# Performance work log

Hardware: AMD Instinct MI355X
Metric: run time of the kernel (lower is better)

Reference implementation:

```python
import jax, jax.numpy as jnp
import numpy as np

N_NODES = 100000
D = 128
R = 4
E = 150000


def setup_inputs() -> dict:
    key = jax.random.key(0)
    k1, k2, k3, k4, k5 = jax.random.split(key, 5)
    x = jax.random.normal(k1, (N_NODES, D), dtype=jnp.float32)
    src_idx = jax.random.randint(k2, (R, E), 0, N_NODES, dtype=jnp.int32)
    dst_idx = jax.random.randint(k3, (R, E), 0, N_NODES, dtype=jnp.int32)
    # xavier-ish scale for weights
    rel_weight = jax.random.normal(k4, (R, D, D), dtype=jnp.float32) * (2.0 / np.sqrt(D))
    loop_weight = jax.random.normal(k5, (D, D), dtype=jnp.float32) * (2.0 / np.sqrt(D))
    h_bias = jnp.zeros((D,), dtype=jnp.float32)
    return {"x": x, "src_idx": src_idx, "dst_idx": dst_idx,
            "rel_weight": rel_weight, "loop_weight": loop_weight, "h_bias": h_bias}


def reference(x, src_idx, dst_idx, rel_weight, loop_weight, h_bias):
    # Per-relation GraphConv with norm='right': gather src feats, scatter-sum to
    # dst, divide by in-degree (clamped to 1), then per-relation linear.
    n = x.shape[0]

    def one_rel(src, dst):
        agg = jax.ops.segment_sum(x[src], dst, num_segments=n)          # [N, D]
        deg = jax.ops.segment_sum(jnp.ones(dst.shape, x.dtype), dst, num_segments=n)
        return agg / jnp.maximum(deg, 1.0)[:, None]

    agg = jax.vmap(one_rel)(src_idx, dst_idx)                           # [R, N, D]
    h = jnp.einsum('rnd,rde->ne', agg, rel_weight)                      # sum over relations
    h = h + x @ loop_weight + h_bias                                    # self-loop + bias
    return jax.nn.relu(h)
```

## Files before the change

### kernel.cpp

```cpp
#include <hip/hip_runtime.h>

#define N_NODES 100000
#define D 128
#define R_REL 4
#define E_EDGES 150000
#define M_SEG (R_REL * N_NODES)
#define NSEG 5
#define CAP 16
#define PLANE ((size_t)N_NODES * D)

typedef _Float16 half8v __attribute__((ext_vector_type(8)));
typedef float f32x4 __attribute__((ext_vector_type(4)));

#define EB ((R_REL * E_EDGES + 255) / 256)
#define BCONV_N (NSEG * 4 * 8 * 64 * 8)
#define BB ((BCONV_N + 255) / 256)
#define XB ((N_NODES * 16 + 255) / 256)

__device__ __forceinline__ void gload_lds16(const void* g, void* l) {
    __builtin_amdgcn_global_load_lds(
        (const __attribute__((address_space(1))) unsigned int*)g,
        (__attribute__((address_space(3))) unsigned int*)l, 16, 0, 0);
}

__global__ __launch_bounds__(256) void prep_kernel(
    const int* __restrict__ src_idx, const int* __restrict__ dst_idx,
    const float* __restrict__ rel_w, const float* __restrict__ loop_w,
    const float* __restrict__ x,
    int* __restrict__ cnt, int* __restrict__ epool,
    _Float16* __restrict__ bh, _Float16* __restrict__ zall)
{
    if (blockIdx.x < EB) {
        int idx = blockIdx.x * 256 + threadIdx.x;
        if (idx >= R_REL * E_EDGES) return;
        int r = idx / E_EDGES;
        int i = r * N_NODES + dst_idx[idx];
        int pos = atomicAdd(&cnt[i], 1);
        if (pos < CAP) epool[(size_t)i * CAP + pos] = src_idx[idx];
    } else if (blockIdx.x < EB + BB) {
        int idx = (blockIdx.x - EB) * 256 + threadIdx.x;
        if (idx >= BCONV_N) return;
        int j   = idx & 7;
        int l   = (idx >> 3) & 63;
        int t   = (idx >> 9) & 7;
        int ks  = (idx >> 12) & 3;
        int seg = idx >> 14;
        int k   = ks * 32 + (l >> 4) * 8 + j;
        int col = t * 16 + (l & 15);
        float v = (seg < R_REL) ? rel_w[((size_t)seg * D + k) * D + col]
                                : loop_w[(size_t)k * D + col];
        bh[idx] = (_Float16)v;
    } else {
        int f = (blockIdx.x - EB - BB) * 256 + threadIdx.x;
        if (f >= N_NODES * 16) return;
        int n = f >> 4;
        int c = f & 15;
        const float4* x4 = (const float4*)x;
        float4 a = x4[(size_t)n * 32 + c * 2];
        float4 b = x4[(size_t)n * 32 + c * 2 + 1];
        half8v h = {(_Float16)a.x, (_Float16)a.y, (_Float16)a.z, (_Float16)a.w,
                    (_Float16)b.x, (_Float16)b.y, (_Float16)b.z, (_Float16)b.w};
        _Float16* xp = zall + (size_t)R_REL * PLANE;
        *(half8v*)(xp + (size_t)n * D + ((c ^ (n & 7)) * 8)) = h;
    }
}

__global__ __launch_bounds__(256) void aggh_kernel(
    const int* __restrict__ cnt,
    const int* __restrict__ epool,
    _Float16* __restrict__ zall)
{
    int idx = blockIdx.x * 256 + threadIdx.x;
    int sid = idx >> 4;
    int lane = idx & 15;
    if (sid >= M_SEG) return;
    int n = sid % N_NODES;

    const _Float16* xp = zall + (size_t)R_REL * PLANE;
    int c = cnt[sid];
    int cc = min(c, CAP);
    int4 i4 = ((const int4*)epool)[(size_t)sid * (CAP / 4)];

    int s0 = (0 < cc) ? i4.x : 0;  float m0 = (0 < cc) ? 1.f : 0.f;
    int s1 = (1 < cc) ? i4.y : 0;  float m1 = (1 < cc) ? 1.f : 0.f;
    int s2 = (2 < cc) ? i4.z : 0;  float m2 = (2 < cc) ? 1.f : 0.f;
    int s3 = (3 < cc) ? i4.w : 0;  float m3 = (3 < cc) ? 1.f : 0.f;
    half8v v0 = *(const half8v*)(xp + (size_t)s0 * D + ((lane ^ (s0 & 7)) * 8));
    half8v v1 = *(const half8v*)(xp + (size_t)s1 * D + ((lane ^ (s1 & 7)) * 8));
    half8v v2 = *(const half8v*)(xp + (size_t)s2 * D + ((lane ^ (s2 & 7)) * 8));
    half8v v3 = *(const half8v*)(xp + (size_t)s3 * D + ((lane ^ (s3 & 7)) * 8));

    float s[8];
    #pragma unroll
    for (int e = 0; e < 8; e++)
        s[e] = (float)v0[e] * m0 + (float)v1[e] * m1 +
               (float)v2[e] * m2 + (float)v3[e] * m3;

    for (int j = 4; j < cc; j++) {
        int sj = epool[(size_t)sid * CAP + j];
        half8v v = *(const half8v*)(xp + (size_t)sj * D + ((lane ^ (sj & 7)) * 8));
        #pragma unroll
        for (int e = 0; e < 8; e++) s[e] += (float)v[e];
    }

    float sc = 1.0f / fmaxf((float)c, 1.0f);
    half8v o;
    #pragma unroll
    for (int e = 0; e < 8; e++) o[e] = (_Float16)(s[e] * sc);
    *(half8v*)(zall + (size_t)sid * D + ((lane ^ (n & 7)) * 8)) = o;
}

__global__ __launch_bounds__(256) void gemm_kernel(
    const _Float16* __restrict__ zall,
    const _Float16* __restrict__ bh,
    const float* __restrict__ bias,
    float* __restrict__ out)
{
    __shared__ __align__(16) char lds[64 * 528];

    int tid = threadIdx.x;
    int w = tid >> 6;
    int l = tid & 63;
    int n0 = blockIdx.x * 64;

    f32x4 acc[8];
    #pragma unroll
    for (int t = 0; t < 8; t++) acc[t] = (f32x4){0.f, 0.f, 0.f, 0.f};

    int arow = w * 16 + (l & 15);

    for (int seg = 0; seg < NSEG; seg++) {
        const char* plane = (const char*)(zall + (size_t)seg * PLANE)
                          + (size_t)n0 * 256;
        #pragma unroll
        for (int p = 0; p < 4; p++) {
            int f = p * 256 + tid;
            gload_lds16(plane + f * 16, lds + f * 16);
        }
        __syncthreads();

        half8v aF[4];
        #pragma unroll
        for (int ks = 0; ks < 4; ks++) {
            int cbyte = (ks * 64 + ((l >> 4) << 4)) ^ ((arow & 7) << 4);
            aF[ks] = *(const half8v*)(lds + arow * 256 + cbyte);
        }
        #pragma unroll
        for (int ks = 0; ks < 4; ks++) {
            size_t fb = ((((size_t)seg * 4 + ks) * 8) * 64 + l) * 8;
            #pragma unroll
            for (int t = 0; t < 8; t++) {
                half8v bF = *(const half8v*)(bh + fb + (size_t)t * 512);
                acc[t] = __builtin_amdgcn_mfma_f32_16x16x32_f16(aF[ks], bF, acc[t], 0, 0, 0);
            }
        }
        __syncthreads();
    }

    int cl = l & 15;
    int lrow0 = w * 16 + ((l >> 4) << 2);
    #pragma unroll
    for (int t = 0; t < 8; t++) {
        float bv = bias[t * 16 + cl];
        #pragma unroll
        for (int reg = 0; reg < 4; reg++) {
            float v = fmaxf(acc[t][reg] + bv, 0.f);
            ((float*)(lds + (lrow0 + reg) * 528))[t * 16 + cl] = v;
        }
    }
    __syncthreads();
    #pragma unroll
    for (int p = 0; p < 8; p++) {
        int f = p * 256 + tid;
        int row = f >> 5;
        int s = f & 31;
        float4 rv = *(const float4*)(lds + row * 528 + s * 16);
        int n = n0 + row;
        if (n < N_NODES)
            *(float4*)((char*)(out + (size_t)n * D) + s * 16) = rv;
    }
}

extern "C" void kernel_launch(void* const* d_in, const int* in_sizes, int n_in,
                              void* d_out, int out_size, void* d_ws, size_t ws_size,
                              hipStream_t stream)
{
    const float* x      = (const float*)d_in[0];
    const int*   src    = (const int*)d_in[1];
    const int*   dst    = (const int*)d_in[2];
    const float* rel_w  = (const float*)d_in[3];
    const float* loop_w = (const float*)d_in[4];
    const float* bias   = (const float*)d_in[5];
    float* out = (float*)d_out;

    int* cnt   = (int*)d_ws;
    int* epool = cnt + M_SEG;
    _Float16* bh = (_Float16*)(epool + (size_t)M_SEG * CAP);
    size_t zoff = ((size_t)M_SEG * 4 + (size_t)M_SEG * CAP * 4 +
                   (size_t)BCONV_N * 2 + 255) & ~(size_t)255;
    _Float16* zall = (_Float16*)((char*)d_ws + zoff);

    hipMemsetAsync(cnt, 0, (size_t)M_SEG * sizeof(int), stream);
    prep_kernel<<<EB + BB + XB, 256, 0, stream>>>(src, dst, rel_w, loop_w, x,
                                                  cnt, epool, bh, zall);

    const int ablocks = (M_SEG * 16) / 256;
    aggh_kernel<<<ablocks, 256, 0, stream>>>(cnt, epool, zall);

    const int gblocks = (N_NODES + 63) / 64;
    gemm_kernel<<<gblocks, 256, 0, stream>>>(zall, bh, bias, out);
}
```

Before: 238.2 us.

## Double-buffer GEMM A tiles, widen block to 128 rows, skip empty segments

The GEMM kernel now handles 128 rows per block, with each wave computing two 16-row tiles that share every loaded B fragment. It prefetches the next segment's A plane into a second LDS buffer while the current one is consumed, so global loads overlap with MFMA work. The epilogue writes its results in two halves through LDS. The aggregation kernel adds an early exit that writes zeros for segments with no edges, which skips the index and gather loads for them. Trade-offs: more LDS and accumulator registers, which can lower occupancy, and half as many GEMM blocks.

Measured after the change: 252.1 us. 5.8% more time.

```diff
diff --git a/kernel.cpp b/kernel.cpp
--- a/kernel.cpp
+++ b/kernel.cpp
@@ -76,12 +76,20 @@
     if (sid >= M_SEG) return;
     int n = sid % N_NODES;
 
+    int c = cnt[sid];
+    _Float16* op = zall + (size_t)sid * D + ((lane ^ (n & 7)) * 8);
+
+    if (c == 0) {
+        half8v o = {};
+        *(half8v*)op = o;
+        return;
+    }
+
     const _Float16* xp = zall + (size_t)R_REL * PLANE;
-    int c = cnt[sid];
     int cc = min(c, CAP);
     int4 i4 = ((const int4*)epool)[(size_t)sid * (CAP / 4)];
 
-    int s0 = (0 < cc) ? i4.x : 0;  float m0 = (0 < cc) ? 1.f : 0.f;
+    int s0 = i4.x;                 float m0 = 1.f;
     int s1 = (1 < cc) ? i4.y : 0;  float m1 = (1 < cc) ? 1.f : 0.f;
     int s2 = (2 < cc) ? i4.z : 0;  float m2 = (2 < cc) ? 1.f : 0.f;
     int s3 = (3 < cc) ? i4.w : 0;  float m3 = (3 < cc) ? 1.f : 0.f;
@@ -103,11 +111,11 @@
         for (int e = 0; e < 8; e++) s[e] += (float)v[e];
     }
 
-    float sc = 1.0f / fmaxf((float)c, 1.0f);
+    float sc = 1.0f / (float)c;
     half8v o;
     #pragma unroll
     for (int e = 0; e < 8; e++) o[e] = (_Float16)(s[e] * sc);
-    *(half8v*)(zall + (size_t)sid * D + ((lane ^ (n & 7)) * 8)) = o;
+    *(half8v*)op = o;
 }
 
 __global__ __launch_bounds__(256) void gemm_kernel(
@@ -116,68 +124,93 @@
     const float* __restrict__ bias,
     float* __restrict__ out)
 {
-    __shared__ __align__(16) char lds[64 * 528];
+    __shared__ __align__(16) char lds[2][32768];
 
     int tid = threadIdx.x;
     int w = tid >> 6;
     int l = tid & 63;
-    int n0 = blockIdx.x * 64;
-
-    f32x4 acc[8];
-    #pragma unroll
-    for (int t = 0; t < 8; t++) acc[t] = (f32x4){0.f, 0.f, 0.f, 0.f};
-
-    int arow = w * 16 + (l & 15);
-
+    int hi = l >> 4;
+    int r15 = l & 15;
+    size_t n0 = (size_t)blockIdx.x * 128;
+
+    f32x4 acc[2][8];
+    #pragma unroll
+    for (int rt = 0; rt < 2; rt++)
+        #pragma unroll
+        for (int t = 0; t < 8; t++) acc[rt][t] = (f32x4){0.f, 0.f, 0.f, 0.f};
+
+    {
+        const char* plane = (const char*)zall + n0 * 256;
+        #pragma unroll
+        for (int p = 0; p < 8; p++) {
+            int f = p * 256 + tid;
+            gload_lds16(plane + (size_t)f * 16, &lds[0][f * 16]);
+        }
+    }
+    __syncthreads();
+
+    int buf = 0;
     for (int seg = 0; seg < NSEG; seg++) {
-        const char* plane = (const char*)(zall + (size_t)seg * PLANE)
-                          + (size_t)n0 * 256;
-        #pragma unroll
-        for (int p = 0; p < 4; p++) {
-            int f = p * 256 + tid;
-            gload_lds16(plane + f * 16, lds + f * 16);
-        }
-        __syncthreads();
-
-        half8v aF[4];
+        if (seg + 1 < NSEG) {
+            const char* plane = (const char*)(zall + (size_t)(seg + 1) * PLANE)
+                              + n0 * 256;
+            #pragma unroll
+            for (int p = 0; p < 8; p++) {
+                int f = p * 256 + tid;
+                gload_lds16(plane + (size_t)f * 16, &lds[buf ^ 1][f * 16]);
+            }
+        }
         #pragma unroll
         for (int ks = 0; ks < 4; ks++) {
-            int cbyte = (ks * 64 + ((l >> 4) << 4)) ^ ((arow & 7) << 4);
-            aF[ks] = *(const half8v*)(lds + arow * 256 + cbyte);
-        }
-        #pragma unroll
-        for (int ks = 0; ks < 4; ks++) {
+            int arow0 = w * 32 + r15;
+            int cb0 = (ks * 64 + (hi << 4)) ^ ((arow0 & 7) << 4);
+            half8v aF0 = *(const half8v*)(&lds[buf][arow0 * 256 + cb0]);
+            int arow1 = arow0 + 16;
+            int cb1 = (ks * 64 + (hi << 4)) ^ ((arow1 & 7) << 4);
+            half8v aF1 = *(const half8v*)(&lds[buf][arow1 * 256 + cb1]);
             size_t fb = ((((size_t)seg * 4 + ks) * 8) * 64 + l) * 8;
             #pragma unroll
             for (int t = 0; t < 8; t++) {
                 half8v bF = *(const half8v*)(bh + fb + (size_t)t * 512);
-                acc[t] = __builtin_amdgcn_mfma_f32_16x16x32_f16(aF[ks], bF, acc[t], 0, 0, 0);
+                acc[0][t] = __builtin_amdgcn_mfma_f32_16x16x32_f16(aF0, bF, acc[0][t], 0, 0, 0);
+                acc[1][t] = __builtin_amdgcn_mfma_f32_16x16x32_f16(aF1, bF, acc[1][t], 0, 0, 0);
             }
         }
         __syncthreads();
-    }
-
-    int cl = l & 15;
-    int lrow0 = w * 16 + ((l >> 4) << 2);
-    #pragma unroll
-    for (int t = 0; t < 8; t++) {
-        float bv = bias[t * 16 + cl];
-        #pragma unroll
-        for (int reg = 0; reg < 4; reg++) {
-            float v = fmaxf(acc[t][reg] + bv, 0.f);
-            ((float*)(lds + (lrow0 + reg) * 528))[t * 16 + cl] = v;
-        }
-    }
-    __syncthreads();
-    #pragma unroll
-    for (int p = 0; p < 8; p++) {
-        int f = p * 256 + tid;
-        int row = f >> 5;
-        int s = f & 31;
-        float4 rv = *(const float4*)(lds + row * 528 + s * 16);
-        int n = n0 + row;
-        if (n < N_NODES)
-            *(float4*)((char*)(out + (size_t)n * D) + s * 16) = rv;
+        buf ^= 1;
+    }
+
+    char* eld = &lds[0][0];
+    int cl = r15;
+    #pragma unroll
+    for (int h = 0; h < 2; h++) {
+        if ((w >> 1) == h) {
+            #pragma unroll
+            for (int rt = 0; rt < 2; rt++) {
+                int lrow0 = w * 32 + rt * 16 + hi * 4 - h * 64;
+                #pragma unroll
+                for (int t = 0; t < 8; t++) {
+                    float bv = bias[t * 16 + cl];
+                    #pragma unroll
+                    for (int reg = 0; reg < 4; reg++) {
+                        float v = fmaxf(acc[rt][t][reg] + bv, 0.f);
+                        ((float*)(eld + (lrow0 + reg) * 528))[t * 16 + cl] = v;
+                    }
+                }
+            }
+        }
+        __syncthreads();
+        #pragma unroll
+        for (int p = 0; p < 8; p++) {
+            int f = p * 256 + tid;
+            int row = f >> 5;
+            int s = f & 31;
+            float4 rv = *(const float4*)(eld + row * 528 + s * 16);
+            size_t n = n0 + h * 64 + row;
+            if (n < N_NODES)
+                *(float4*)((char*)(out + n * D) + s * 16) = rv;
+        }
+        __syncthreads();
     }
 }
 
@@ -207,6 +240,6 @@
     const int ablocks = (M_SEG * 16) / 256;
     aggh_kernel<<<ablocks, 256, 0, stream>>>(cnt, epool, zall);
 
-    const int gblocks = (N_NODES + 63) / 64;
+    const int gblocks = (N_NODES + 127) / 128;
     gemm_kernel<<<gblocks, 256, 0, stream>>>(zall, bh, bias, out);
 }
```
